# Kernel optimization log

Hardware: AMD Instinct MI355X
Metric: run time of the kernel (lower is better)

## Reference

```python
import jax, jax.numpy as jnp
import numpy as np

SAMPLE_RATE = 44100
NUM_FILTERS = 3
FREQ_LO, FREQ_HI = 100.0, 3000.0
Q_LO, Q_HI = 1.0, 5.0
GAIN_LO, GAIN_HI = -24.0, 24.0


def _center_freqs():
    # power_ratio(i/N, f_lo, f_hi) = f_lo * (f_hi/f_lo)**(i/N)
    return [FREQ_LO * (FREQ_HI / FREQ_LO) ** (i / NUM_FILTERS) for i in range(NUM_FILTERS)]


def setup_inputs() -> dict:
    key = jax.random.key(0)
    k1, k2, k3 = jax.random.split(key, 3)
    audio = jax.random.normal(k1, (32, 441000), dtype=jnp.float32)  # [B, T]
    # Q sampled like power_ratio(u, q_lo, q_hi) = q_lo*(q_hi/q_lo)**u
    u = jax.random.uniform(k2, (NUM_FILTERS,), dtype=jnp.float32)
    qs = Q_LO * (Q_HI / Q_LO) ** u
    gains = jax.random.uniform(k3, (NUM_FILTERS,), dtype=jnp.float32,
                               minval=GAIN_LO, maxval=GAIN_HI)
    return {"audio": audio, "qs": qs, "gains": gains}


def _biquad(x, b0, b1, b2, a1, a2):
    """Direct-form-I biquad over time axis. x: [B, T]; coeffs normalized by a0."""
    B = x.shape[0]
    z = jnp.zeros((B,), x.dtype)

    def step(carry, xn):
        x1, x2, y1, y2 = carry
        yn = b0 * xn + b1 * x1 + b2 * x2 - a1 * y1 - a2 * y2
        return (xn, x1, yn, y1), yn

    _, y = jax.lax.scan(step, (z, z, z, z), x.T)  # scan over T
    return y.T


def _peaking_eq(audio, center_freq, gain, Q):
    # torchaudio.functional.equalizer_biquad coefficients
    w0 = 2.0 * jnp.pi * center_freq / SAMPLE_RATE
    alpha = jnp.sin(w0) / (2.0 * Q)
    A = jnp.exp(gain / 40.0 * jnp.log(10.0))  # 10**(gain/40)
    b0 = 1.0 + alpha * A
    b1 = -2.0 * jnp.cos(w0)
    b2 = 1.0 - alpha * A
    a0 = 1.0 + alpha / A
    a1 = -2.0 * jnp.cos(w0)
    a2 = 1.0 - alpha / A
    return _biquad(audio, b0 / a0, b1 / a0, b2 / a0, a1 / a0, a2 / a0)


def reference(audio, qs, gains):
    cfs = _center_freqs()
    for i in range(NUM_FILTERS):
        audio = _peaking_eq(audio, cfs[i], gains[i], qs[i])
    return audio
```

## Files before the change

### kernel.cpp

```cpp
#include <hip/hip_runtime.h>
#include <math.h>

#define SR      44100.0
#define T_LEN   441000
#define B_ROWS  32
#define NCH     13782
#define GCH     (B_ROWS * NCH)
#define BPR     54
#define NBLK    (B_ROWS * BPR)
#define NMAT    14

#define WS_MAT  0
#define WS_AG   512
#define WS_O    10880
#define WS_F    21248

typedef __attribute__((address_space(1))) const void gconst_t;
typedef __attribute__((address_space(3))) void lds_t;
#define GL2LDS(gp, lp) __builtin_amdgcn_global_load_lds((gconst_t*)(gp), (lds_t*)(lp), 16, 0, 0)


#define COMPUTE_COEFS(scoef, dco, qs, gains) do { \
    if (threadIdx.x < 3) { \
      int f = threadIdx.x; \
      double cfq = 100.0 * exp(log(30.0) * (double)f / 3.0); \
      double w0 = 2.0 * M_PI * cfq / SR; \
      double alpha = sin(w0) / (2.0 * (double)qs[f]); \
      double Ag = exp((double)gains[f] * (2.302585092994045684 / 40.0)); \
      double a0 = 1.0 + alpha / Ag; \
      double c0 = (1.0 + alpha * Ag) / a0; \
      double c1 = (-2.0 * cos(w0)) / a0; \
      double c2 = (1.0 - alpha * Ag) / a0; \
      double c3 = c1; \
      double c4 = (1.0 - alpha / Ag) / a0; \
      if (dco) { double* dc = (double*)(dco); \
        dc[f*5+0]=c0; dc[f*5+1]=c1; dc[f*5+2]=c2; dc[f*5+3]=c3; dc[f*5+4]=c4; } \
      scoef[f*5+0]=(float)c0; scoef[f*5+1]=(float)c1; scoef[f*5+2]=(float)c2; \
      scoef[f*5+3]=(float)c3; scoef[f*5+4]=(float)c4; \
    } \
  } while (0)

#define LOAD_COEFS(cf) \
  const float b00=cf[0],b10=cf[1],b20=cf[2],a10=cf[3],a20=cf[4]; \
  const float b01=cf[5],b11=cf[6],b21=cf[7],a11=cf[8],a21=cf[9]; \
  const float b02=cf[10],b12=cf[11],b22=cf[12],a12=cf[13],a22=cf[14];

#define CASCADE_STEP(xx) do { \
    float y1 = fmaf(b00, (xx), s11); \
    s11 = fmaf(-a10, y1, fmaf(b10, (xx), s21)); \
    s21 = fmaf(-a20, y1, b20 * (xx)); \
    float y2 = fmaf(b01, y1, s12); \
    s12 = fmaf(-a11, y2, fmaf(b11, y1, s22)); \
    s22 = fmaf(-a21, y2, b21 * y1); \
    y3 = fmaf(b02, y2, s13); \
    s13 = fmaf(-a12, y3, fmaf(b12, y2, s23)); \
    s23 = fmaf(-a22, y3, b22 * y2); \
  } while (0)

#define MV6(dst, M, v, add) do { \
    _Pragma("unroll") \
    for (int _i = 0; _i < 6; _i++) { \
      float _s = (add)[_i]; \
      _Pragma("unroll") \
      for (int _k = 0; _k < 6; _k++) _s = fmaf((M)[_i*6+_k], (v)[_k], _s); \
      (dst)[_i] = _s; \
    } \
  } while (0)

__device__ __forceinline__ void mm6d(const double* X, const double* Y, double* Z, int t) {
  if (t < 36) {
    int i = t / 6, j = t % 6;
    double s = 0.0;
    #pragma unroll
    for (int k = 0; k < 6; k++) s += X[i*6+k] * Y[k*6+j];
    Z[t] = s;
  }
}



__global__ __launch_bounds__(256) void kA_scan(const float* __restrict__ x,
                                               const float* __restrict__ qs,
                                               const float* __restrict__ gains,
                                               float* __restrict__ ws) {
  __shared__ __align__(16) float lds[4 * 2048];
  __shared__ double Da[36], Db[36];
  __shared__ double dco[15];
  __shared__ float sVm[NMAT][36];
  __shared__ float scoef[16];
  const int tid = threadIdx.x;
  const int wib = tid >> 6, lane = tid & 63;
  const int b = blockIdx.x;
  const int row = b / BPR, jb = b - row * BPR;
  const int wci = (jb << 2) + wib;
  long rowbase = (long)row * T_LEN;
  int s0 = wci << 11;
  int span4 = (min(2048, T_LEN - s0)) >> 2;
  const float4* xp = (const float4*)(x + rowbase + s0);
  float* slab = lds + (wib << 11);
  if (span4 == 512) {
    #pragma unroll
    for (int i = 0; i < 8; i++) {
      int s = (i << 6) + lane;
      int g = (s & ~7) | ((s & 7) ^ ((s >> 3) & 7));
      GL2LDS(xp + g, slab + (i << 8));
    }
  } else {
    #pragma unroll
    for (int i = 0; i < 8; i++) {
      int s = (i << 6) + lane;
      int g = (s & ~7) | ((s & 7) ^ ((s >> 3) & 7));
      if (g < span4) GL2LDS(xp + g, slab + (i << 8));
    }
  }
  COMPUTE_COEFS(scoef, dco, qs, gains);
  if (wib == 0) {
    if (lane == 0) {
      double u[7] = {0,0,0,0,0,0,1};
      for (int f = 0; f < 3; f++) {
        double c0=dco[f*5+0], c1=dco[f*5+1], c2=dco[f*5+2], c3=dco[f*5+3], c4=dco[f*5+4];
        double yv[7], s1p[7], s2p[7];
        for (int i = 0; i < 7; i++) {
          yv[i]  = c0 * u[i] + ((i == 2*f)   ? 1.0 : 0.0);
          s1p[i] = c1 * u[i] + ((i == 2*f+1) ? 1.0 : 0.0) - c3 * yv[i];
          s2p[i] = c2 * u[i] - c4 * yv[i];
        }
        for (int i = 0; i < 6; i++) { Da[(2*f)*6+i] = s1p[i]; Da[(2*f+1)*6+i] = s2p[i]; }
        for (int i = 0; i < 7; i++) u[i] = yv[i];
      }
    }
    double* cur = Da; double* oth = Db;
    #pragma unroll
    for (int s = 0; s < 5; s++) {
      mm6d(cur, cur, oth, lane);
      double* tm = cur; cur = oth; oth = tm;
    }
    #pragma unroll
    for (int k = 0; k < NMAT; k++) {
      if (lane < 36) {
        float wv = (float)cur[lane];
        sVm[k][lane] = wv;
        if (b == 0) ws[WS_MAT + k*36 + lane] = wv;
      }
      if (k < NMAT - 1) {
        mm6d(cur, cur, oth, lane);
        double* tm = cur; cur = oth; oth = tm;
      }
    }
  }
  __syncthreads();

  int ci = (jb << 8) + tid;
  bool valid = ci < NCH;
  float f[6] = {0,0,0,0,0,0};
  if (valid) {
    LOAD_COEFS(scoef);
    int rem = min(32, T_LEN - (ci << 5));
    int n4 = rem >> 2;
    const float* rowp = slab + (lane << 5);
    int xr = lane & 7;
    float s11=0,s21=0,s12=0,s22=0,s13=0,s23=0, y3;
    if (n4 == 8) {
      #pragma unroll
      for (int j4 = 0; j4 < 8; j4++) {
        float4 v = *(const float4*)(rowp + ((j4 ^ xr) << 2));
        CASCADE_STEP(v.x); CASCADE_STEP(v.y); CASCADE_STEP(v.z); CASCADE_STEP(v.w);
      }
    } else {
      for (int j4 = 0; j4 < n4; j4++) {
        float4 v = *(const float4*)(rowp + ((j4 ^ xr) << 2));
        CASCADE_STEP(v.x); CASCADE_STEP(v.y); CASCADE_STEP(v.z); CASCADE_STEP(v.w);
      }
    }
    (void)y3;
    f[0]=s11; f[1]=s21; f[2]=s12; f[3]=s22; f[4]=s13; f[5]=s23;
  }
  __syncthreads();

  float* src = lds;
  float* dst = lds + 1792;
  #pragma unroll
  for (int i = 0; i < 6; i++) src[tid*7 + i] = f[i];
  __syncthreads();
  for (int k = 0; k < 8; k++) {
    int d = 1 << k;
    float nv[6];
    if (tid >= d) { MV6(nv, sVm[k], src + (tid-d)*7, src + tid*7); }
    else {
      #pragma unroll
      for (int i = 0; i < 6; i++) nv[i] = src[tid*7 + i];
    }
    #pragma unroll
    for (int i = 0; i < 6; i++) dst[tid*7 + i] = nv[i];
    __syncthreads();
    float* tm = src; src = dst; dst = tm;
  }
  if (valid) {
    float e[6];
    if (tid > 0) {
      #pragma unroll
      for (int i = 0; i < 6; i++) e[i] = src[(tid-1)*7 + i];
    } else {
      #pragma unroll
      for (int i = 0; i < 6; i++) e[i] = 0.0f;
    }
    float2* E = (float2*)(ws + WS_F + ((long)row * NCH + ci) * 6);
    E[0] = make_float2(e[0], e[1]); E[1] = make_float2(e[2], e[3]); E[2] = make_float2(e[4], e[5]);
  }
  if (tid == 255 && jb < BPR - 1) {
    #pragma unroll
    for (int i = 0; i < 6; i++) ws[WS_AG + ((long)row * BPR + jb) * 6 + i] = src[255*7 + i];
  }
}


__global__ __launch_bounds__(64) void kB_off(float* __restrict__ ws) {
  int row = blockIdx.x, j = threadIdx.x;
  __shared__ float sB[6][36];
  __shared__ float buf[2][64][7];
  for (int i = j; i < 216; i += 64) sB[i/36][i%36] = ws[WS_MAT + (8 + i/36)*36 + (i%36)];
  float v[6] = {0,0,0,0,0,0};
  if (j < BPR - 1) {
    #pragma unroll
    for (int i = 0; i < 6; i++) v[i] = ws[WS_AG + ((long)row * BPR + j) * 6 + i];
  }
  __syncthreads();
  #pragma unroll
  for (int i = 0; i < 6; i++) buf[0][j][i] = v[i];
  __syncthreads();
  int cur = 0;
  for (int k = 0; k < 6; k++) {
    int d = 1 << k;
    float nv[6];
    if (j >= d) { MV6(nv, sB[k], buf[cur][j-d], buf[cur][j]); }
    else {
      #pragma unroll
      for (int i = 0; i < 6; i++) nv[i] = buf[cur][j][i];
    }
    #pragma unroll
    for (int i = 0; i < 6; i++) buf[cur^1][j][i] = nv[i];
    __syncthreads();
    cur ^= 1;
  }
  if (j < BPR) {
    float o[6];
    if (j > 0) {
      #pragma unroll
      for (int i = 0; i < 6; i++) o[i] = buf[cur][j-1][i];
    } else {
      #pragma unroll
      for (int i = 0; i < 6; i++) o[i] = 0.0f;
    }
    #pragma unroll
    for (int i = 0; i < 6; i++) ws[WS_O + ((long)row * BPR + j) * 6 + i] = o[i];
  }
}


__global__ __launch_bounds__(256) void kC_emit(const float* __restrict__ x,
                                               const float* __restrict__ qs,
                                               const float* __restrict__ gains,
                                               float* __restrict__ y,
                                               const float* __restrict__ ws) {
  __shared__ __align__(16) float lds[4 * 2048];
  __shared__ float scoef[16];
  __shared__ float smat[288];
  const int tid = threadIdx.x;
  const int wib = tid >> 6, lane = tid & 63;
  const int b = blockIdx.x;
  const int row = b / BPR, jb = b - row * BPR;
  const int wci = (jb << 2) + wib;
  long rowbase = (long)row * T_LEN;
  int s0 = wci << 11;
  int span4 = (min(2048, T_LEN - s0)) >> 2;
  const float4* xp = (const float4*)(x + rowbase + s0);
  float* slab = lds + (wib << 11);
  if (span4 == 512) {
    #pragma unroll
    for (int i = 0; i < 8; i++) {
      int s = (i << 6) + lane;
      int g = (s & ~7) | ((s & 7) ^ ((s >> 3) & 7));
      GL2LDS(xp + g, slab + (i << 8));
    }
  } else {
    #pragma unroll
    for (int i = 0; i < 8; i++) {
      int s = (i << 6) + lane;
      int g = (s & ~7) | ((s & 7) ^ ((s >> 3) & 7));
      if (g < span4) GL2LDS(xp + g, slab + (i << 8));
    }
  }
  for (int i = tid; i < 288; i += 256) smat[i] = ws[WS_MAT + i];
  COMPUTE_COEFS(scoef, (double*)nullptr, qs, gains);
  float o6[6];
  {
    const float* Op = ws + WS_O + ((long)row * BPR + jb) * 6;
    #pragma unroll
    for (int i = 0; i < 6; i++) o6[i] = Op[i];
  }
  int ci = (jb << 8) + tid;
  bool valid = ci < NCH;
  float e0=0,e1v=0,e2=0,e3=0,e4=0,e5=0;
  if (valid) {
    const float2* E = (const float2*)(ws + WS_F + ((long)row * NCH + ci) * 6);
    float2 p0 = E[0], p1 = E[1], p2 = E[2];
    e0=p0.x; e1v=p0.y; e2=p1.x; e3=p1.y; e4=p2.x; e5=p2.y;
  }
  __syncthreads();
  if (valid) {
    LOAD_COEFS(scoef);
    float m[6];
    #pragma unroll
    for (int i = 0; i < 6; i++) m[i] = o6[i];
    float z6[6] = {0,0,0,0,0,0};
    #pragma unroll
    for (int k = 0; k < 8; k++) {
      if ((tid >> k) & 1) {
        float nm[6];
        MV6(nm, smat + k*36, m, z6);
        #pragma unroll
        for (int i = 0; i < 6; i++) m[i] = nm[i];
      }
    }
    float s11=e0+m[0], s21=e1v+m[1], s12=e2+m[2], s22=e3+m[3], s13=e4+m[4], s23=e5+m[5];
    int rem = min(32, T_LEN - (ci << 5));
    int n4 = rem >> 2;
    float* rowp = slab + (lane << 5);
    int xr = lane & 7;
    float y3;
    if (n4 == 8) {
      #pragma unroll
      for (int j4 = 0; j4 < 8; j4++) {
        float* p = rowp + ((j4 ^ xr) << 2);
        float4 v = *(const float4*)p;
        float4 o;
        CASCADE_STEP(v.x); o.x = y3;
        CASCADE_STEP(v.y); o.y = y3;
        CASCADE_STEP(v.z); o.z = y3;
        CASCADE_STEP(v.w); o.w = y3;
        *(float4*)p = o;
      }
    } else {
      for (int j4 = 0; j4 < n4; j4++) {
        float* p = rowp + ((j4 ^ xr) << 2);
        float4 v = *(const float4*)p;
        float4 o;
        CASCADE_STEP(v.x); o.x = y3;
        CASCADE_STEP(v.y); o.y = y3;
        CASCADE_STEP(v.z); o.z = y3;
        CASCADE_STEP(v.w); o.w = y3;
        *(float4*)p = o;
      }
    }
  }
  __syncthreads();
  float4* yp = (float4*)(y + rowbase + s0);
  if (span4 == 512) {
    #pragma unroll
    for (int i = 0; i < 8; i++) {
      int g = (i << 6) + lane;
      int s = (g & ~7) | ((g & 7) ^ ((g >> 3) & 7));
      yp[g] = *(const float4*)(slab + (s << 2));
    }
  } else {
    #pragma unroll
    for (int i = 0; i < 8; i++) {
      int g = (i << 6) + lane;
      int s = (g & ~7) | ((g & 7) ^ ((g >> 3) & 7));
      if (g < span4) yp[g] = *(const float4*)(slab + (s << 2));
    }
  }
}

extern "C" void kernel_launch(void* const* d_in, const int* in_sizes, int n_in,
                              void* d_out, int out_size, void* d_ws, size_t ws_size,
                              hipStream_t stream) {
  const float* audio = (const float*)d_in[0];
  const float* qs    = (const float*)d_in[1];
  const float* gains = (const float*)d_in[2];
  float* out = (float*)d_out;
  float* ws  = (float*)d_ws;

  hipLaunchKernelGGL(kA_scan, dim3(NBLK), dim3(256), 0, stream, audio, qs, gains, ws);
  hipLaunchKernelGGL(kB_off, dim3(B_ROWS), dim3(64), 0, stream, ws);
  hipLaunchKernelGGL(kC_emit, dim3(NBLK), dim3(256), 0, stream, audio, qs, gains, out, ws);
}
```

Before: 62.61 us.

## Fuse three-kernel scan into single-pass decoupled look-back kernel

```diff
diff --git a/kernel.cpp b/kernel.cpp
--- a/kernel.cpp
+++ b/kernel.cpp
@@ -5,19 +5,18 @@
 #define T_LEN   441000
 #define B_ROWS  32
 #define NCH     13782
-#define GCH     (B_ROWS * NCH)
 #define BPR     54
 #define NBLK    (B_ROWS * BPR)
-#define NMAT    14
-
-#define WS_MAT  0
-#define WS_AG   512
-#define WS_O    10880
-#define WS_F    21248
+#define NMAT    9
+
+#define WS_AG   2048
+#define WS_INC  12416
 
 typedef __attribute__((address_space(1))) const void gconst_t;
 typedef __attribute__((address_space(3))) void lds_t;
 #define GL2LDS(gp, lp) __builtin_amdgcn_global_load_lds((gconst_t*)(gp), (lds_t*)(lp), 16, 0, 0)
+
+#define AGENT __HIP_MEMORY_SCOPE_AGENT
 
 
 #define COMPUTE_COEFS(scoef, dco, qs, gains) do { \
@@ -33,8 +32,7 @@
       double c2 = (1.0 - alpha * Ag) / a0; \
       double c3 = c1; \
       double c4 = (1.0 - alpha / Ag) / a0; \
-      if (dco) { double* dc = (double*)(dco); \
-        dc[f*5+0]=c0; dc[f*5+1]=c1; dc[f*5+2]=c2; dc[f*5+3]=c3; dc[f*5+4]=c4; } \
+      dco[f*5+0]=c0; dco[f*5+1]=c1; dco[f*5+2]=c2; dco[f*5+3]=c3; dco[f*5+4]=c4; \
       scoef[f*5+0]=(float)c0; scoef[f*5+1]=(float)c1; scoef[f*5+2]=(float)c2; \
       scoef[f*5+3]=(float)c3; scoef[f*5+4]=(float)c4; \
     } \
@@ -78,20 +76,32 @@
 }
 
 
-
-__global__ __launch_bounds__(256) void kA_scan(const float* __restrict__ x,
-                                               const float* __restrict__ qs,
-                                               const float* __restrict__ gains,
-                                               float* __restrict__ ws) {
+__global__ __launch_bounds__(256) void fused(const float* __restrict__ x,
+                                             const float* __restrict__ qs,
+                                             const float* __restrict__ gains,
+                                             float* __restrict__ y,
+                                             float* __restrict__ ws) {
   __shared__ __align__(16) float lds[4 * 2048];
-  __shared__ double Da[36], Db[36];
-  __shared__ double dco[15];
+  __shared__ double Da[36], Db[36], dco[15];
   __shared__ float sVm[NMAT][36];
   __shared__ float scoef[16];
+  __shared__ float wtot[4][6];
+  __shared__ float sO[6];
+  __shared__ float gstack[54][6];
+  __shared__ int sTick;
   const int tid = threadIdx.x;
   const int wib = tid >> 6, lane = tid & 63;
-  const int b = blockIdx.x;
-  const int row = b / BPR, jb = b - row * BPR;
+
+  unsigned int* flags = (unsigned int*)ws + 16;
+  float* AGp  = ws + WS_AG;
+  float* INCp = ws + WS_INC;
+
+  if (tid == 0)
+    sTick = __hip_atomic_fetch_add((int*)ws, 1, __ATOMIC_RELAXED, AGENT);
+  __syncthreads();
+  const int vbid = sTick;
+  const int row = vbid / BPR, jb = vbid - row * BPR;
+
   const int wci = (jb << 2) + wib;
   long rowbase = (long)row * T_LEN;
   int s0 = wci << 11;
@@ -137,11 +147,7 @@
     }
     #pragma unroll
     for (int k = 0; k < NMAT; k++) {
-      if (lane < 36) {
-        float wv = (float)cur[lane];
-        sVm[k][lane] = wv;
-        if (b == 0) ws[WS_MAT + k*36 + lane] = wv;
-      }
+      if (lane < 36) sVm[k][lane] = (float)cur[lane];
       if (k < NMAT - 1) {
         mm6d(cur, cur, oth, lane);
         double* tm = cur; cur = oth; oth = tm;
@@ -152,179 +158,162 @@
 
   int ci = (jb << 8) + tid;
   bool valid = ci < NCH;
-  float f[6] = {0,0,0,0,0,0};
+  float f6[6] = {0,0,0,0,0,0};
+  {
+    LOAD_COEFS(scoef);
+    if (valid) {
+      int n4 = (ci == NCH - 1) ? 2 : 8;
+      const float* rowp = slab + (lane << 5);
+      int xr = lane & 7;
+      float s11=0,s21=0,s12=0,s22=0,s13=0,s23=0, y3;
+      if (n4 == 8) {
+        #pragma unroll
+        for (int j4 = 0; j4 < 8; j4++) {
+          float4 v = *(const float4*)(rowp + ((j4 ^ xr) << 2));
+          CASCADE_STEP(v.x); CASCADE_STEP(v.y); CASCADE_STEP(v.z); CASCADE_STEP(v.w);
+        }
+      } else {
+        for (int j4 = 0; j4 < 2; j4++) {
+          float4 v = *(const float4*)(rowp + ((j4 ^ xr) << 2));
+          CASCADE_STEP(v.x); CASCADE_STEP(v.y); CASCADE_STEP(v.z); CASCADE_STEP(v.w);
+        }
+      }
+      (void)y3;
+      f6[0]=s11; f6[1]=s21; f6[2]=s12; f6[3]=s22; f6[4]=s13; f6[5]=s23;
+    }
+  }
+
+  float v6[6];
+  #pragma unroll
+  for (int i = 0; i < 6; i++) v6[i] = f6[i];
+  #pragma unroll
+  for (int k = 0; k < 6; k++) {
+    int d = 1 << k;
+    float u[6];
+    #pragma unroll
+    for (int i = 0; i < 6; i++) u[i] = __shfl_up(v6[i], d, 64);
+    float nv[6];
+    MV6(nv, sVm[k], u, v6);
+    #pragma unroll
+    for (int i = 0; i < 6; i++) v6[i] = (lane >= d) ? nv[i] : v6[i];
+  }
+  float ex[6];
+  #pragma unroll
+  for (int i = 0; i < 6; i++) {
+    float t = __shfl_up(v6[i], 1, 64);
+    ex[i] = (lane > 0) ? t : 0.0f;
+  }
+  if (lane == 63) {
+    #pragma unroll
+    for (int i = 0; i < 6; i++) wtot[wib][i] = v6[i];
+  }
+  __syncthreads();
+
+  if (wib == 0) {
+    float g6[6];
+    if (lane == 0) {
+      #pragma unroll
+      for (int i = 0; i < 6; i++) g6[i] = wtot[0][i];
+      #pragma unroll
+      for (int w = 1; w < 4; w++) {
+        float ng[6];
+        MV6(ng, sVm[6], g6, wtot[w]);
+        #pragma unroll
+        for (int i = 0; i < 6; i++) g6[i] = ng[i];
+      }
+      #pragma unroll
+      for (int i = 0; i < 6; i++)
+        __hip_atomic_store(&AGp[(long)vbid*6+i], g6[i], __ATOMIC_RELAXED, AGENT);
+      __hip_atomic_store(&flags[vbid], 1u, __ATOMIC_RELEASE, AGENT);
+    }
+    if (jb == 0) {
+      if (lane == 0) {
+        #pragma unroll
+        for (int i = 0; i < 6; i++) {
+          sO[i] = 0.0f;
+          __hip_atomic_store(&INCp[(long)vbid*6+i], g6[i], __ATOMIC_RELAXED, AGENT);
+        }
+        __hip_atomic_store(&flags[vbid], 2u, __ATOMIC_RELEASE, AGENT);
+      }
+    } else {
+      int l = lane;
+      int pred = vbid - 1 - l;
+      int l_inc;
+      unsigned int fl;
+      while (true) {
+        fl = (l < jb) ? __hip_atomic_load(&flags[pred], __ATOMIC_ACQUIRE, AGENT) : 2u;
+        unsigned long long b2 = __ballot(fl == 2u);
+        l_inc = (int)(__ffsll((long long)b2) - 1);
+        unsigned long long b1 = __ballot(fl >= 1u);
+        unsigned long long need = (l_inc >= 64) ? ~0ull : ((1ull << l_inc) - 1ull);
+        if ((b1 & need) == need) break;
+        __builtin_amdgcn_s_sleep(2);
+      }
+      if (l < l_inc) {
+        #pragma unroll
+        for (int i = 0; i < 6; i++)
+          gstack[l][i] = __hip_atomic_load(&AGp[(long)pred*6+i], __ATOMIC_RELAXED, AGENT);
+      } else if (l == l_inc && l < jb) {
+        #pragma unroll
+        for (int i = 0; i < 6; i++)
+          gstack[l][i] = __hip_atomic_load(&INCp[(long)pred*6+i], __ATOMIC_RELAXED, AGENT);
+      }
+      if (lane == 0) {
+        float v[6];
+        if (l_inc == jb) {
+          #pragma unroll
+          for (int i = 0; i < 6; i++) v[i] = 0.0f;
+        } else {
+          #pragma unroll
+          for (int i = 0; i < 6; i++) v[i] = gstack[l_inc][i];
+        }
+        for (int l2 = l_inc - 1; l2 >= 0; --l2) {
+          float nv[6];
+          MV6(nv, sVm[8], v, gstack[l2]);
+          #pragma unroll
+          for (int i = 0; i < 6; i++) v[i] = nv[i];
+        }
+        #pragma unroll
+        for (int i = 0; i < 6; i++) sO[i] = v[i];
+        float inc[6];
+        MV6(inc, sVm[8], v, g6);
+        #pragma unroll
+        for (int i = 0; i < 6; i++)
+          __hip_atomic_store(&INCp[(long)vbid*6+i], inc[i], __ATOMIC_RELAXED, AGENT);
+        __hip_atomic_store(&flags[vbid], 2u, __ATOMIC_RELEASE, AGENT);
+      }
+    }
+  }
+  __syncthreads();
+
+  float wabs[6];
+  #pragma unroll
+  for (int i = 0; i < 6; i++) wabs[i] = sO[i];
+  for (int w = 0; w < wib; w++) {
+    float nv[6];
+    MV6(nv, sVm[6], wabs, wtot[w]);
+    #pragma unroll
+    for (int i = 0; i < 6; i++) wabs[i] = nv[i];
+  }
+  float m[6];
+  #pragma unroll
+  for (int i = 0; i < 6; i++) m[i] = wabs[i];
+  float z6[6] = {0,0,0,0,0,0};
+  #pragma unroll
+  for (int k = 0; k < 6; k++) {
+    if ((lane >> k) & 1) {
+      float nm[6];
+      MV6(nm, sVm[k], m, z6);
+      #pragma unroll
+      for (int i = 0; i < 6; i++) m[i] = nm[i];
+    }
+  }
+
   if (valid) {
     LOAD_COEFS(scoef);
-    int rem = min(32, T_LEN - (ci << 5));
-    int n4 = rem >> 2;
-    const float* rowp = slab + (lane << 5);
-    int xr = lane & 7;
-    float s11=0,s21=0,s12=0,s22=0,s13=0,s23=0, y3;
-    if (n4 == 8) {
-      #pragma unroll
-      for (int j4 = 0; j4 < 8; j4++) {
-        float4 v = *(const float4*)(rowp + ((j4 ^ xr) << 2));
-        CASCADE_STEP(v.x); CASCADE_STEP(v.y); CASCADE_STEP(v.z); CASCADE_STEP(v.w);
-      }
-    } else {
-      for (int j4 = 0; j4 < n4; j4++) {
-        float4 v = *(const float4*)(rowp + ((j4 ^ xr) << 2));
-        CASCADE_STEP(v.x); CASCADE_STEP(v.y); CASCADE_STEP(v.z); CASCADE_STEP(v.w);
-      }
-    }
-    (void)y3;
-    f[0]=s11; f[1]=s21; f[2]=s12; f[3]=s22; f[4]=s13; f[5]=s23;
-  }
-  __syncthreads();
-
-  float* src = lds;
-  float* dst = lds + 1792;
-  #pragma unroll
-  for (int i = 0; i < 6; i++) src[tid*7 + i] = f[i];
-  __syncthreads();
-  for (int k = 0; k < 8; k++) {
-    int d = 1 << k;
-    float nv[6];
-    if (tid >= d) { MV6(nv, sVm[k], src + (tid-d)*7, src + tid*7); }
-    else {
-      #pragma unroll
-      for (int i = 0; i < 6; i++) nv[i] = src[tid*7 + i];
-    }
-    #pragma unroll
-    for (int i = 0; i < 6; i++) dst[tid*7 + i] = nv[i];
-    __syncthreads();
-    float* tm = src; src = dst; dst = tm;
-  }
-  if (valid) {
-    float e[6];
-    if (tid > 0) {
-      #pragma unroll
-      for (int i = 0; i < 6; i++) e[i] = src[(tid-1)*7 + i];
-    } else {
-      #pragma unroll
-      for (int i = 0; i < 6; i++) e[i] = 0.0f;
-    }
-    float2* E = (float2*)(ws + WS_F + ((long)row * NCH + ci) * 6);
-    E[0] = make_float2(e[0], e[1]); E[1] = make_float2(e[2], e[3]); E[2] = make_float2(e[4], e[5]);
-  }
-  if (tid == 255 && jb < BPR - 1) {
-    #pragma unroll
-    for (int i = 0; i < 6; i++) ws[WS_AG + ((long)row * BPR + jb) * 6 + i] = src[255*7 + i];
-  }
-}
-
-
-__global__ __launch_bounds__(64) void kB_off(float* __restrict__ ws) {
-  int row = blockIdx.x, j = threadIdx.x;
-  __shared__ float sB[6][36];
-  __shared__ float buf[2][64][7];
-  for (int i = j; i < 216; i += 64) sB[i/36][i%36] = ws[WS_MAT + (8 + i/36)*36 + (i%36)];
-  float v[6] = {0,0,0,0,0,0};
-  if (j < BPR - 1) {
-    #pragma unroll
-    for (int i = 0; i < 6; i++) v[i] = ws[WS_AG + ((long)row * BPR + j) * 6 + i];
-  }
-  __syncthreads();
-  #pragma unroll
-  for (int i = 0; i < 6; i++) buf[0][j][i] = v[i];
-  __syncthreads();
-  int cur = 0;
-  for (int k = 0; k < 6; k++) {
-    int d = 1 << k;
-    float nv[6];
-    if (j >= d) { MV6(nv, sB[k], buf[cur][j-d], buf[cur][j]); }
-    else {
-      #pragma unroll
-      for (int i = 0; i < 6; i++) nv[i] = buf[cur][j][i];
-    }
-    #pragma unroll
-    for (int i = 0; i < 6; i++) buf[cur^1][j][i] = nv[i];
-    __syncthreads();
-    cur ^= 1;
-  }
-  if (j < BPR) {
-    float o[6];
-    if (j > 0) {
-      #pragma unroll
-      for (int i = 0; i < 6; i++) o[i] = buf[cur][j-1][i];
-    } else {
-      #pragma unroll
-      for (int i = 0; i < 6; i++) o[i] = 0.0f;
-    }
-    #pragma unroll
-    for (int i = 0; i < 6; i++) ws[WS_O + ((long)row * BPR + j) * 6 + i] = o[i];
-  }
-}
-
-
-__global__ __launch_bounds__(256) void kC_emit(const float* __restrict__ x,
-                                               const float* __restrict__ qs,
-                                               const float* __restrict__ gains,
-                                               float* __restrict__ y,
-                                               const float* __restrict__ ws) {
-  __shared__ __align__(16) float lds[4 * 2048];
-  __shared__ float scoef[16];
-  __shared__ float smat[288];
-  const int tid = threadIdx.x;
-  const int wib = tid >> 6, lane = tid & 63;
-  const int b = blockIdx.x;
-  const int row = b / BPR, jb = b - row * BPR;
-  const int wci = (jb << 2) + wib;
-  long rowbase = (long)row * T_LEN;
-  int s0 = wci << 11;
-  int span4 = (min(2048, T_LEN - s0)) >> 2;
-  const float4* xp = (const float4*)(x + rowbase + s0);
-  float* slab = lds + (wib << 11);
-  if (span4 == 512) {
-    #pragma unroll
-    for (int i = 0; i < 8; i++) {
-      int s = (i << 6) + lane;
-      int g = (s & ~7) | ((s & 7) ^ ((s >> 3) & 7));
-      GL2LDS(xp + g, slab + (i << 8));
-    }
-  } else {
-    #pragma unroll
-    for (int i = 0; i < 8; i++) {
-      int s = (i << 6) + lane;
-      int g = (s & ~7) | ((s & 7) ^ ((s >> 3) & 7));
-      if (g < span4) GL2LDS(xp + g, slab + (i << 8));
-    }
-  }
-  for (int i = tid; i < 288; i += 256) smat[i] = ws[WS_MAT + i];
-  COMPUTE_COEFS(scoef, (double*)nullptr, qs, gains);
-  float o6[6];
-  {
-    const float* Op = ws + WS_O + ((long)row * BPR + jb) * 6;
-    #pragma unroll
-    for (int i = 0; i < 6; i++) o6[i] = Op[i];
-  }
-  int ci = (jb << 8) + tid;
-  bool valid = ci < NCH;
-  float e0=0,e1v=0,e2=0,e3=0,e4=0,e5=0;
-  if (valid) {
-    const float2* E = (const float2*)(ws + WS_F + ((long)row * NCH + ci) * 6);
-    float2 p0 = E[0], p1 = E[1], p2 = E[2];
-    e0=p0.x; e1v=p0.y; e2=p1.x; e3=p1.y; e4=p2.x; e5=p2.y;
-  }
-  __syncthreads();
-  if (valid) {
-    LOAD_COEFS(scoef);
-    float m[6];
-    #pragma unroll
-    for (int i = 0; i < 6; i++) m[i] = o6[i];
-    float z6[6] = {0,0,0,0,0,0};
-    #pragma unroll
-    for (int k = 0; k < 8; k++) {
-      if ((tid >> k) & 1) {
-        float nm[6];
-        MV6(nm, smat + k*36, m, z6);
-        #pragma unroll
-        for (int i = 0; i < 6; i++) m[i] = nm[i];
-      }
-    }
-    float s11=e0+m[0], s21=e1v+m[1], s12=e2+m[2], s22=e3+m[3], s13=e4+m[4], s23=e5+m[5];
-    int rem = min(32, T_LEN - (ci << 5));
-    int n4 = rem >> 2;
+    float s11=ex[0]+m[0], s21=ex[1]+m[1], s12=ex[2]+m[2],
+          s22=ex[3]+m[3], s13=ex[4]+m[4], s23=ex[5]+m[5];
+    int n4 = (ci == NCH - 1) ? 2 : 8;
     float* rowp = slab + (lane << 5);
     int xr = lane & 7;
     float y3;
@@ -341,7 +330,7 @@
         *(float4*)p = o;
       }
     } else {
-      for (int j4 = 0; j4 < n4; j4++) {
+      for (int j4 = 0; j4 < 2; j4++) {
         float* p = rowp + ((j4 ^ xr) << 2);
         float4 v = *(const float4*)p;
         float4 o;
@@ -381,7 +370,6 @@
   float* out = (float*)d_out;
   float* ws  = (float*)d_ws;
 
-  hipLaunchKernelGGL(kA_scan, dim3(NBLK), dim3(256), 0, stream, audio, qs, gains, ws);
-  hipLaunchKernelGGL(kB_off, dim3(B_ROWS), dim3(64), 0, stream, ws);
-  hipLaunchKernelGGL(kC_emit, dim3(NBLK), dim3(256), 0, stream, audio, qs, gains, out, ws);
+  hipMemsetAsync(d_ws, 0, 7040, stream);
+  hipLaunchKernelGGL(fused, dim3(NBLK), dim3(256), 0, stream, audio, qs, gains, out, ws);
 }
```

Result: slower. 131.9 us (+110.7%).

## Fold block-offset scan into emit kernel with wavefront shuffles, dropping middle launch

Applied to the files above, without the earlier changes.

```diff
diff --git a/kernel.cpp b/kernel.cpp
--- a/kernel.cpp
+++ b/kernel.cpp
@@ -12,7 +12,6 @@
 
 #define WS_MAT  0
 #define WS_AG   512
-#define WS_O    10880
 #define WS_F    21248
 
 typedef __attribute__((address_space(1))) const void gconst_t;
@@ -33,8 +32,7 @@
       double c2 = (1.0 - alpha * Ag) / a0; \
       double c3 = c1; \
       double c4 = (1.0 - alpha / Ag) / a0; \
-      if (dco) { double* dc = (double*)(dco); \
-        dc[f*5+0]=c0; dc[f*5+1]=c1; dc[f*5+2]=c2; dc[f*5+3]=c3; dc[f*5+4]=c4; } \
+      dco[f*5+0]=c0; dco[f*5+1]=c1; dco[f*5+2]=c2; dco[f*5+3]=c3; dco[f*5+4]=c4; \
       scoef[f*5+0]=(float)c0; scoef[f*5+1]=(float)c1; scoef[f*5+2]=(float)c2; \
       scoef[f*5+3]=(float)c3; scoef[f*5+4]=(float)c4; \
     } \
@@ -77,6 +75,24 @@
   }
 }
 
+
+#define STAGE_AUDIO() do { \
+    if (span4 == 512) { \
+      _Pragma("unroll") \
+      for (int i = 0; i < 8; i++) { \
+        int s = (i << 6) + lane; \
+        int g = (s & ~7) | ((s & 7) ^ ((s >> 3) & 7)); \
+        GL2LDS(xp + g, slab + (i << 8)); \
+      } \
+    } else { \
+      _Pragma("unroll") \
+      for (int i = 0; i < 8; i++) { \
+        int s = (i << 6) + lane; \
+        int g = (s & ~7) | ((s & 7) ^ ((s >> 3) & 7)); \
+        if (g < span4) GL2LDS(xp + g, slab + (i << 8)); \
+      } \
+    } \
+  } while (0)
 
 
 __global__ __launch_bounds__(256) void kA_scan(const float* __restrict__ x,
@@ -98,21 +114,7 @@
   int span4 = (min(2048, T_LEN - s0)) >> 2;
   const float4* xp = (const float4*)(x + rowbase + s0);
   float* slab = lds + (wib << 11);
-  if (span4 == 512) {
-    #pragma unroll
-    for (int i = 0; i < 8; i++) {
-      int s = (i << 6) + lane;
-      int g = (s & ~7) | ((s & 7) ^ ((s >> 3) & 7));
-      GL2LDS(xp + g, slab + (i << 8));
-    }
-  } else {
-    #pragma unroll
-    for (int i = 0; i < 8; i++) {
-      int s = (i << 6) + lane;
-      int g = (s & ~7) | ((s & 7) ^ ((s >> 3) & 7));
-      if (g < span4) GL2LDS(xp + g, slab + (i << 8));
-    }
-  }
+  STAGE_AUDIO();
   COMPUTE_COEFS(scoef, dco, qs, gains);
   if (wib == 0) {
     if (lane == 0) {
@@ -152,11 +154,10 @@
 
   int ci = (jb << 8) + tid;
   bool valid = ci < NCH;
-  float f[6] = {0,0,0,0,0,0};
+  float f6[6] = {0,0,0,0,0,0};
   if (valid) {
     LOAD_COEFS(scoef);
-    int rem = min(32, T_LEN - (ci << 5));
-    int n4 = rem >> 2;
+    int n4 = (ci == NCH - 1) ? 2 : 8;
     const float* rowp = slab + (lane << 5);
     int xr = lane & 7;
     float s11=0,s21=0,s12=0,s22=0,s13=0,s23=0, y3;
@@ -167,20 +168,20 @@
         CASCADE_STEP(v.x); CASCADE_STEP(v.y); CASCADE_STEP(v.z); CASCADE_STEP(v.w);
       }
     } else {
-      for (int j4 = 0; j4 < n4; j4++) {
+      for (int j4 = 0; j4 < 2; j4++) {
         float4 v = *(const float4*)(rowp + ((j4 ^ xr) << 2));
         CASCADE_STEP(v.x); CASCADE_STEP(v.y); CASCADE_STEP(v.z); CASCADE_STEP(v.w);
       }
     }
     (void)y3;
-    f[0]=s11; f[1]=s21; f[2]=s12; f[3]=s22; f[4]=s13; f[5]=s23;
+    f6[0]=s11; f6[1]=s21; f6[2]=s12; f6[3]=s22; f6[4]=s13; f6[5]=s23;
   }
   __syncthreads();
 
   float* src = lds;
   float* dst = lds + 1792;
   #pragma unroll
-  for (int i = 0; i < 6; i++) src[tid*7 + i] = f[i];
+  for (int i = 0; i < 6; i++) src[tid*7 + i] = f6[i];
   __syncthreads();
   for (int k = 0; k < 8; k++) {
     int d = 1 << k;
@@ -210,49 +211,6 @@
   if (tid == 255 && jb < BPR - 1) {
     #pragma unroll
     for (int i = 0; i < 6; i++) ws[WS_AG + ((long)row * BPR + jb) * 6 + i] = src[255*7 + i];
-  }
-}
-
-
-__global__ __launch_bounds__(64) void kB_off(float* __restrict__ ws) {
-  int row = blockIdx.x, j = threadIdx.x;
-  __shared__ float sB[6][36];
-  __shared__ float buf[2][64][7];
-  for (int i = j; i < 216; i += 64) sB[i/36][i%36] = ws[WS_MAT + (8 + i/36)*36 + (i%36)];
-  float v[6] = {0,0,0,0,0,0};
-  if (j < BPR - 1) {
-    #pragma unroll
-    for (int i = 0; i < 6; i++) v[i] = ws[WS_AG + ((long)row * BPR + j) * 6 + i];
-  }
-  __syncthreads();
-  #pragma unroll
-  for (int i = 0; i < 6; i++) buf[0][j][i] = v[i];
-  __syncthreads();
-  int cur = 0;
-  for (int k = 0; k < 6; k++) {
-    int d = 1 << k;
-    float nv[6];
-    if (j >= d) { MV6(nv, sB[k], buf[cur][j-d], buf[cur][j]); }
-    else {
-      #pragma unroll
-      for (int i = 0; i < 6; i++) nv[i] = buf[cur][j][i];
-    }
-    #pragma unroll
-    for (int i = 0; i < 6; i++) buf[cur^1][j][i] = nv[i];
-    __syncthreads();
-    cur ^= 1;
-  }
-  if (j < BPR) {
-    float o[6];
-    if (j > 0) {
-      #pragma unroll
-      for (int i = 0; i < 6; i++) o[i] = buf[cur][j-1][i];
-    } else {
-      #pragma unroll
-      for (int i = 0; i < 6; i++) o[i] = 0.0f;
-    }
-    #pragma unroll
-    for (int i = 0; i < 6; i++) ws[WS_O + ((long)row * BPR + j) * 6 + i] = o[i];
   }
 }
 
@@ -263,8 +221,10 @@
                                                float* __restrict__ y,
                                                const float* __restrict__ ws) {
   __shared__ __align__(16) float lds[4 * 2048];
+  __shared__ float smat[NMAT * 36];
   __shared__ float scoef[16];
-  __shared__ float smat[288];
+  __shared__ double dco[15];
+  __shared__ float sO[6];
   const int tid = threadIdx.x;
   const int wib = tid >> 6, lane = tid & 63;
   const int b = blockIdx.x;
@@ -275,28 +235,18 @@
   int span4 = (min(2048, T_LEN - s0)) >> 2;
   const float4* xp = (const float4*)(x + rowbase + s0);
   float* slab = lds + (wib << 11);
-  if (span4 == 512) {
-    #pragma unroll
-    for (int i = 0; i < 8; i++) {
-      int s = (i << 6) + lane;
-      int g = (s & ~7) | ((s & 7) ^ ((s >> 3) & 7));
-      GL2LDS(xp + g, slab + (i << 8));
-    }
-  } else {
-    #pragma unroll
-    for (int i = 0; i < 8; i++) {
-      int s = (i << 6) + lane;
-      int g = (s & ~7) | ((s & 7) ^ ((s >> 3) & 7));
-      if (g < span4) GL2LDS(xp + g, slab + (i << 8));
-    }
-  }
-  for (int i = tid; i < 288; i += 256) smat[i] = ws[WS_MAT + i];
-  COMPUTE_COEFS(scoef, (double*)nullptr, qs, gains);
-  float o6[6];
-  {
-    const float* Op = ws + WS_O + ((long)row * BPR + jb) * 6;
-    #pragma unroll
-    for (int i = 0; i < 6; i++) o6[i] = Op[i];
+  STAGE_AUDIO();
+  for (int i = tid; i < NMAT * 36; i += 256) smat[i] = ws[WS_MAT + i];
+  float ag[6] = {0,0,0,0,0,0};
+  if (wib == 0 && lane < BPR - 1) {
+    const float* p = ws + WS_AG + ((long)row * BPR + lane) * 6;
+    #pragma unroll
+    for (int i = 0; i < 6; i++) ag[i] = p[i];
+  }
+  COMPUTE_COEFS(scoef, dco, qs, gains);
+  if (tid == 0 && jb == 0) {
+    #pragma unroll
+    for (int i = 0; i < 6; i++) sO[i] = 0.0f;
   }
   int ci = (jb << 8) + tid;
   bool valid = ci < NCH;
@@ -307,11 +257,34 @@
     e0=p0.x; e1v=p0.y; e2=p1.x; e3=p1.y; e4=p2.x; e5=p2.y;
   }
   __syncthreads();
+
+  if (wib == 0 && jb > 0) {
+    float v6s[6];
+    #pragma unroll
+    for (int i = 0; i < 6; i++) v6s[i] = ag[i];
+    #pragma unroll
+    for (int k = 0; k < 6; k++) {
+      int d = 1 << k;
+      float u[6];
+      #pragma unroll
+      for (int i = 0; i < 6; i++) u[i] = __shfl_up(v6s[i], d, 64);
+      float nv[6];
+      MV6(nv, smat + (8 + k) * 36, u, v6s);
+      #pragma unroll
+      for (int i = 0; i < 6; i++) v6s[i] = (lane >= d) ? nv[i] : v6s[i];
+    }
+    if (lane == jb - 1) {
+      #pragma unroll
+      for (int i = 0; i < 6; i++) sO[i] = v6s[i];
+    }
+  }
+  __syncthreads();
+
   if (valid) {
     LOAD_COEFS(scoef);
     float m[6];
     #pragma unroll
-    for (int i = 0; i < 6; i++) m[i] = o6[i];
+    for (int i = 0; i < 6; i++) m[i] = sO[i];
     float z6[6] = {0,0,0,0,0,0};
     #pragma unroll
     for (int k = 0; k < 8; k++) {
@@ -323,8 +296,7 @@
       }
     }
     float s11=e0+m[0], s21=e1v+m[1], s12=e2+m[2], s22=e3+m[3], s13=e4+m[4], s23=e5+m[5];
-    int rem = min(32, T_LEN - (ci << 5));
-    int n4 = rem >> 2;
+    int n4 = (ci == NCH - 1) ? 2 : 8;
     float* rowp = slab + (lane << 5);
     int xr = lane & 7;
     float y3;
@@ -341,7 +313,7 @@
         *(float4*)p = o;
       }
     } else {
-      for (int j4 = 0; j4 < n4; j4++) {
+      for (int j4 = 0; j4 < 2; j4++) {
         float* p = rowp + ((j4 ^ xr) << 2);
         float4 v = *(const float4*)p;
         float4 o;
@@ -382,6 +354,5 @@
   float* ws  = (float*)d_ws;
 
   hipLaunchKernelGGL(kA_scan, dim3(NBLK), dim3(256), 0, stream, audio, qs, gains, ws);
-  hipLaunchKernelGGL(kB_off, dim3(B_ROWS), dim3(64), 0, stream, ws);
   hipLaunchKernelGGL(kC_emit, dim3(NBLK), dim3(256), 0, stream, audio, qs, gains, out, ws);
 }
```

New measurement: 59.96 us. 1.04x faster.
